# Optimization experiments

Measured on AMD Instinct MI355X. Metric: run time of the kernel, lower is better.

The kernel has to match this reference:

```python
import jax, jax.numpy as jnp
import numpy as np

SR = 48000
MIN_MIDI, MAX_MIDI = 30.0, 60.0
MIN_ALPHA, MAX_ALPHA = 0.2, 3.0
MIN_W, MAX_W = 100.0, 8000.0
MIN_Q, MAX_Q = 0.7071, 8.0
NOTE_ON_DUR = 0.125
OSC_SHAPE = 1.0
OSC_GAIN = 0.5
DIST_GAIN = 1.0
N = 524288


def setup_inputs() -> dict:
    key = jax.random.key(0)
    ks = jax.random.split(key, 5)
    return {
        "x": jax.random.normal(ks[0], (1, N), dtype=jnp.float32),
        "midi_f0_0to1": jax.random.uniform(ks[1], (1,), dtype=jnp.float32),
        "alpha_0to1": jax.random.uniform(ks[2], (1,), dtype=jnp.float32),
        "w_mod_sig": jax.random.uniform(ks[3], (1, N), dtype=jnp.float32),
        "q_mod_sig": jax.random.uniform(ks[4], (1, N), dtype=jnp.float32),
        "phase": jnp.zeros((1, 1), dtype=jnp.float32),
        "zi": jnp.zeros((1, 2), dtype=jnp.float32),
    }


def _tv_biquad(x, b, a, zi):
    # Time-varying biquad, direct-form II transposed.
    # x: [n], b: [n,3] (b0,b1,b2 normalized), a: [n,2] (a1,a2 normalized), zi: [2]
    def step(carry, inp):
        s1, s2 = carry
        xt, bt, at = inp
        y = bt[0] * xt + s1
        s1 = bt[1] * xt - at[0] * y + s2
        s2 = bt[2] * xt - at[1] * y
        return (s1, s2), y

    _, y = jax.lax.scan(step, (zi[0], zi[1]), (x, b, a))
    return y


def reference(x, midi_f0_0to1, alpha_0to1, w_mod_sig, q_mod_sig, phase, zi):
    n = x.shape[-1]
    # --- control mapping ---
    alpha = alpha_0to1 * (MAX_ALPHA - MIN_ALPHA) + MIN_ALPHA          # [1]
    midi_f0 = jnp.round(midi_f0_0to1 * (MAX_MIDI - MIN_MIDI) + MIN_MIDI)
    f0_hz = 440.0 * 2.0 ** ((midi_f0 - 69.0) / 12.0)                  # [1]
    t = jnp.arange(n, dtype=jnp.float32)
    # --- decaying note-on envelope raised to learned alpha ---
    env = jnp.clip(1.0 - t / (NOTE_ON_DUR * SR), 0.0, 1.0) ** alpha   # [n]
    # --- phase-accumulating saw/square morph oscillator ---
    arg = phase[0, 0] + 2.0 * jnp.pi * f0_hz * t / SR                 # [n]
    ph = jnp.mod(arg / (2.0 * jnp.pi), 1.0)
    saw = 2.0 * ph - 1.0
    sq = jnp.where(ph < 0.5, 1.0, -1.0)
    dry = OSC_GAIN * (OSC_SHAPE * sq + (1.0 - OSC_SHAPE) * saw) * env  # [n]
    # --- per-sample RBJ lowpass biquad coefficients ---
    w_hz = w_mod_sig[0] * (MAX_W - MIN_W) + MIN_W                     # [n]
    q = q_mod_sig[0] * (MAX_Q - MIN_Q) + MIN_Q                        # [n]
    w0 = 2.0 * jnp.pi * w_hz / SR
    cw, sw = jnp.cos(w0), jnp.sin(w0)
    af = sw / (2.0 * q)
    a0 = 1.0 + af
    b = jnp.stack([(1.0 - cw) / 2.0, 1.0 - cw, (1.0 - cw) / 2.0], axis=-1) / a0[:, None]
    a = jnp.stack([-2.0 * cw, 1.0 - af], axis=-1) / a0[:, None]
    # --- sequential time-varying filter + distortion ---
    y_a = _tv_biquad(dry, b, a, zi[0])                                # [n]
    wet = jnp.tanh(DIST_GAIN * y_a)[None, :]                          # [1, n]
    return wet
```

## Files before the change

### kernel.cpp

```cpp
#include <hip/hip_runtime.h>
#include <math.h>


#define LCHUNK 16

struct Aff { float m00,m01,m10,m11,c0,c1; };

__device__ __forceinline__ Aff aff_identity(){ return Aff{1.f,0.f,0.f,1.f,0.f,0.f}; }

__device__ __forceinline__ Aff aff_compose(const Aff& B, const Aff& A){
  Aff r;
  r.m00 = fmaf(B.m00, A.m00, B.m01*A.m10);
  r.m01 = fmaf(B.m00, A.m01, B.m01*A.m11);
  r.m10 = fmaf(B.m10, A.m00, B.m11*A.m10);
  r.m11 = fmaf(B.m10, A.m01, B.m11*A.m11);
  r.c0  = fmaf(B.m00, A.c0, fmaf(B.m01, A.c1, B.c0));
  r.c1  = fmaf(B.m10, A.c0, fmaf(B.m11, A.c1, B.c1));
  return r;
}

__device__ __forceinline__ Aff aff_shfl_up(const Aff& a, int delta){
  Aff r;
  r.m00 = __shfl_up(a.m00, delta, 64);
  r.m01 = __shfl_up(a.m01, delta, 64);
  r.m10 = __shfl_up(a.m10, delta, 64);
  r.m11 = __shfl_up(a.m11, delta, 64);
  r.c0  = __shfl_up(a.c0 , delta, 64);
  r.c1  = __shfl_up(a.c1 , delta, 64);
  return r;
}

__device__ __forceinline__ void coefs(float wv, float qv,
                                      float& na1, float& na2, float& b0, float& b1){
  float rev = fmaf(wv, 7900.0f/48000.0f, 100.0f/48000.0f);
  float cw = __builtin_amdgcn_cosf(rev);
  float sw = __builtin_amdgcn_sinf(rev);
  float qq = fmaf(qv, 8.0f - 0.7071f, 0.7071f);
  float af = sw * (0.5f * __builtin_amdgcn_rcpf(qq));
  float ia = __builtin_amdgcn_rcpf(1.0f + af);
  float t1 = 1.0f - cw;
  b1 = t1 * ia;
  b0 = 0.5f * b1;
  na1 = (cw + cw) * ia;
  na2 = (af - 1.0f) * ia;
}

__device__ __forceinline__ void get_controls(const float* midi01, const float* alpha01,
                                             const float* phasep,
                                             float& alpha, float& f0c, float& phase0){
  #pragma clang fp contract(off)
  alpha = alpha01[0]*2.8f + 0.2f;
  float md = rintf(midi01[0]*30.0f + 30.0f);
  float f0 = 440.0f * exp2f((md - 69.0f)/12.0f);
  f0c = 6.2831855f * f0;
  phase0 = phasep[0];
}

__device__ __forceinline__ float osc_dry(int i, float alpha, float f0c, float phase0){
  #pragma clang fp contract(off)
  float tf = (float)i;
  float u = 1.0f - tf/6000.0f;
  u = fminf(fmaxf(u, 0.0f), 1.0f);
  float env = powf(u, alpha);
  float arg = phase0 + (f0c*tf)/48000.0f;
  float d = arg/6.2831855f;
  float m = d - floorf(d);
  float sq = (m < 0.5f) ? 1.0f : -1.0f;
  return (0.5f*sq)*env;
}

__global__ __launch_bounds__(256) void k_pass1(const float* __restrict__ w,
    const float* __restrict__ qm, const float* __restrict__ midi01,
    const float* __restrict__ alpha01, const float* __restrict__ phasep,
    float4* __restrict__ Pf4, float2* __restrict__ Pf2, float4* __restrict__ Bt){
  const int tid = threadIdx.x;
  const int g = blockIdx.x*256 + tid;
  const int base = g * LCHUNK;
  float m00=1.f, m01=0.f, m10=0.f, m11=1.f, c0=0.f, c1=0.f;
  const bool has_dry = (base < 6000);
  float alpha=0.f, f0c=0.f, phase0=0.f;
  if (has_dry) get_controls(midi01, alpha01, phasep, alpha, f0c, phase0);
  const float4* w4p = reinterpret_cast<const float4*>(w + base);
  const float4* q4p = reinterpret_cast<const float4*>(qm + base);
  #pragma unroll
  for (int j=0;j<LCHUNK/4;j++){
    float4 w4 = w4p[j];
    float4 q4 = q4p[j];
    #pragma unroll
    for (int e=0;e<4;e++){
      float na1,na2,b0,b1;
      coefs((&w4.x)[e], (&q4.x)[e], na1,na2,b0,b1);
      float nm00 = fmaf(na1, m00, m10);
      float nm01 = fmaf(na1, m01, m11);
      m10 = na2*m00; m11 = na2*m01;
      m00 = nm00;   m01 = nm01;
      float nc0 = fmaf(na1, c0, c1);
      float nc1 = na2*c0;
      if (has_dry){
        float x = osc_dry(base + j*4 + e, alpha, f0c, phase0);
        nc0 = fmaf(fmaf(na1,b0,b1), x, nc0);
        nc1 = fmaf(fmaf(na2,b0,b0), x, nc1);
      }
      c0 = nc0; c1 = nc1;
    }
  }
  const int lane = tid & 63, wv = tid >> 6;
  Aff Tin{m00,m01,m10,m11,c0,c1};
  #pragma unroll
  for (int off=1; off<64; off<<=1){
    Aff P = aff_shfl_up(Tin, off);
    if (lane >= off) Tin = aff_compose(Tin, P);
  }
  __shared__ float wt[4][6];
  if (lane == 63){
    wt[wv][0]=Tin.m00; wt[wv][1]=Tin.m01; wt[wv][2]=Tin.m10;
    wt[wv][3]=Tin.m11; wt[wv][4]=Tin.c0;  wt[wv][5]=Tin.c1;
  }
  __syncthreads();
  Aff Wp = aff_identity();
  for (int j=0;j<wv;j++){
    Aff Wj{wt[j][0],wt[j][1],wt[j][2],wt[j][3],wt[j][4],wt[j][5]};
    Wp = aff_compose(Wj, Wp);
  }
  Aff Ex = aff_shfl_up(Tin, 1);
  if (lane == 0) Ex = aff_identity();
  Aff Epre = aff_compose(Ex, Wp);
  Pf4[g] = make_float4(Epre.m00, Epre.m01, Epre.m10, Epre.m11);
  Pf2[g] = make_float2(Epre.c0, Epre.c1);
  if (tid == 255){
    Aff Full = aff_compose(Tin, Wp);
    Bt[blockIdx.x*2+0] = make_float4(Full.m00, Full.m01, Full.m10, Full.m11);
    Bt[blockIdx.x*2+1] = make_float4(Full.c0, Full.c1, 0.f, 0.f);
  }
}

__global__ __launch_bounds__(256) void k_pass2(const float* __restrict__ w,
    const float* __restrict__ qm, const float* __restrict__ midi01,
    const float* __restrict__ alpha01, const float* __restrict__ phasep,
    const float* __restrict__ zi,
    const float4* __restrict__ Pf4, const float2* __restrict__ Pf2,
    const float4* __restrict__ Bt, float* __restrict__ out, int B){
  const int tid = threadIdx.x;
  const int blk = blockIdx.x;
  const int lane = tid & 63;
  __shared__ float2 stsh[128];
  __shared__ float wtot[6];
  const float z0 = zi[0], z1 = zi[1];
  if (tid < 128){
    Aff T = aff_identity();
    if (tid < B){
      float4 A4 = Bt[tid*2+0];
      float4 C4 = Bt[tid*2+1];
      T = Aff{A4.x,A4.y,A4.z,A4.w,C4.x,C4.y};
    }
    #pragma unroll
    for (int off=1; off<64; off<<=1){
      Aff P = aff_shfl_up(T, off);
      if (lane >= off) T = aff_compose(T, P);
    }
    if (tid == 63){
      wtot[0]=T.m00; wtot[1]=T.m01; wtot[2]=T.m10;
      wtot[3]=T.m11; wtot[4]=T.c0;  wtot[5]=T.c1;
    }
    __syncthreads();
    if (tid >= 64){
      Aff W0{wtot[0],wtot[1],wtot[2],wtot[3],wtot[4],wtot[5]};
      T = aff_compose(T, W0);
    }
    float s0 = fmaf(T.m00, z0, fmaf(T.m01, z1, T.c0));
    float s1 = fmaf(T.m10, z0, fmaf(T.m11, z1, T.c1));
    stsh[tid] = make_float2(s0, s1);
  } else {
    __syncthreads();
  }
  __syncthreads();
  const float2 e = (blk == 0) ? make_float2(z0, z1) : stsh[blk-1];
  const int g = blk*256 + tid;
  const int base = g * LCHUNK;
  float4 P4 = Pf4[g];
  float2 P2 = Pf2[g];
  float u1 = fmaf(P4.x, e.x, fmaf(P4.y, e.y, P2.x));
  float u2 = fmaf(P4.z, e.x, fmaf(P4.w, e.y, P2.y));
  const bool has_dry = (base < 6000);
  float alpha=0.f, f0c=0.f, phase0=0.f;
  if (has_dry) get_controls(midi01, alpha01, phasep, alpha, f0c, phase0);
  const float4* w4p = reinterpret_cast<const float4*>(w + base);
  const float4* q4p = reinterpret_cast<const float4*>(qm + base);
  float4* o4p = reinterpret_cast<float4*>(out + base);
  #pragma unroll
  for (int j=0;j<LCHUNK/4;j++){
    float4 w4 = w4p[j];
    float4 q4 = q4p[j];
    float4 ov;
    #pragma unroll
    for (int ecnt=0;ecnt<4;ecnt++){
      float na1,na2,b0,b1;
      coefs((&w4.x)[ecnt], (&q4.x)[ecnt], na1,na2,b0,b1);
      float x = 0.0f;
      if (has_dry) x = osc_dry(base + j*4 + ecnt, alpha, f0c, phase0);
      float y = fmaf(b0, x, u1);
      float nu1 = fmaf(b1, x, fmaf(na1, y, u2));
      float nu2 = fmaf(b0, x, na2*y);
      u1 = nu1; u2 = nu2;
      float ey = __expf(y + y);
      float r = __builtin_amdgcn_rcpf(ey + 1.0f);
      (&ov.x)[ecnt] = fmaf(-2.0f, r, 1.0f);
    }
    o4p[j] = ov;
  }
}

__global__ void k_naive(const float* __restrict__ w, const float* __restrict__ qm,
    const float* __restrict__ midi01, const float* __restrict__ alpha01,
    const float* __restrict__ phasep, const float* __restrict__ zi,
    float* __restrict__ out, int n){
  if (blockIdx.x != 0 || threadIdx.x != 0) return;
  float alpha,f0c,phase0; get_controls(midi01, alpha01, phasep, alpha, f0c, phase0);
  float u1 = zi[0], u2 = zi[1];
  for (int i=0;i<n;i++){
    float na1,na2,b0,b1;
    coefs(w[i], qm[i], na1,na2,b0,b1);
    float x = (i < 6000) ? osc_dry(i, alpha, f0c, phase0) : 0.0f;
    float y = fmaf(b0, x, u1);
    float nu1 = fmaf(b1, x, fmaf(na1, y, u2));
    float nu2 = fmaf(b0, x, na2*y);
    u1 = nu1; u2 = nu2;
    float ey = __expf(y + y);
    float r = __builtin_amdgcn_rcpf(ey + 1.0f);
    out[i] = fmaf(-2.0f, r, 1.0f);
  }
}

extern "C" void kernel_launch(void* const* d_in, const int* in_sizes, int n_in,
                              void* d_out, int out_size, void* d_ws, size_t ws_size,
                              hipStream_t stream) {
  const float* midi01  = (const float*)d_in[1];
  const float* alpha01 = (const float*)d_in[2];
  const float* w       = (const float*)d_in[3];
  const float* qm      = (const float*)d_in[4];
  const float* ph      = (const float*)d_in[5];
  const float* zi      = (const float*)d_in[6];
  float* out = (float*)d_out;
  const int n = in_sizes[0];
  const int G = n / LCHUNK;
  const int B = G / 256;
  const size_t pf4_bytes = (size_t)G * sizeof(float4);
  const size_t pf2_bytes = (size_t)G * sizeof(float2);
  const size_t bt_bytes  = (size_t)B * 2 * sizeof(float4);
  const size_t need = pf4_bytes + pf2_bytes + bt_bytes;

  if ((n % LCHUNK) != 0 || (G % 256) != 0 || B > 128 || ws_size < need) {
    k_naive<<<1, 64, 0, stream>>>(w, qm, midi01, alpha01, ph, zi, out, n);
    return;
  }
  float4* Pf4 = (float4*)d_ws;
  float2* Pf2 = (float2*)((char*)d_ws + pf4_bytes);
  float4* Bt  = (float4*)((char*)d_ws + pf4_bytes + pf2_bytes);

  k_pass1<<<dim3(B), dim3(256), 0, stream>>>(w, qm, midi01, alpha01, ph, Pf4, Pf2, Bt);
  k_pass2<<<dim3(B), dim3(256), 0, stream>>>(w, qm, midi01, alpha01, ph, zi,
                                             Pf4, Pf2, Bt, out, B);
}
```

Baseline: 87.75 us.

## Fuse two-pass biquad scan into one cooperative kernel with grid sync

Merges the two scan passes into one cooperative kernel. Per-sample coefficients and oscillator samples stay in registers across a grid.sync, so the second pass no longer reloads w/q, recomputes coefs and osc_dry, or round-trips per-thread prefix transforms through global memory. The cost is a cooperative launch with a grid-wide barrier and higher register pressure from 64 cached floats per thread. If the cooperative launch fails, it falls back to the serial naive kernel.

```diff
diff --git a/kernel.cpp b/kernel.cpp
--- a/kernel.cpp
+++ b/kernel.cpp
@@ -1,8 +1,12 @@
 #include <hip/hip_runtime.h>
+#include <hip/hip_cooperative_groups.h>
 #include <math.h>
 
 
+namespace cg = cooperative_groups;
+
 #define LCHUNK 16
+#define NBLK 128
 
 struct Aff { float m00,m01,m10,m11,c0,c1; };
 
@@ -31,7 +35,7 @@
 }
 
 __device__ __forceinline__ void coefs(float wv, float qv,
-                                      float& na1, float& na2, float& b0, float& b1){
+                                      float& na1, float& na2, float& b0){
   float rev = fmaf(wv, 7900.0f/48000.0f, 100.0f/48000.0f);
   float cw = __builtin_amdgcn_cosf(rev);
   float sw = __builtin_amdgcn_sinf(rev);
@@ -39,8 +43,7 @@
   float af = sw * (0.5f * __builtin_amdgcn_rcpf(qq));
   float ia = __builtin_amdgcn_rcpf(1.0f + af);
   float t1 = 1.0f - cw;
-  b1 = t1 * ia;
-  b0 = 0.5f * b1;
+  b0 = 0.5f * (t1 * ia);
   na1 = (cw + cw) * ia;
   na2 = (af - 1.0f) * ia;
 }
@@ -69,42 +72,56 @@
   return (0.5f*sq)*env;
 }
 
-__global__ __launch_bounds__(256) void k_pass1(const float* __restrict__ w,
+__global__ __launch_bounds__(256) void k_fused(const float* __restrict__ w,
     const float* __restrict__ qm, const float* __restrict__ midi01,
     const float* __restrict__ alpha01, const float* __restrict__ phasep,
-    float4* __restrict__ Pf4, float2* __restrict__ Pf2, float4* __restrict__ Bt){
+    const float* __restrict__ zi, float4* __restrict__ Bt,
+    float* __restrict__ out){
+  cg::grid_group grid = cg::this_grid();
   const int tid = threadIdx.x;
-  const int g = blockIdx.x*256 + tid;
+  const int blk = blockIdx.x;
+  const int lane = tid & 63, wv = tid >> 6;
+  const int g = blk*256 + tid;
   const int base = g * LCHUNK;
-  float m00=1.f, m01=0.f, m10=0.f, m11=1.f, c0=0.f, c1=0.f;
+
+  float na1s[LCHUNK], na2s[LCHUNK], b0s[LCHUNK], xs[LCHUNK];
   const bool has_dry = (base < 6000);
   float alpha=0.f, f0c=0.f, phase0=0.f;
   if (has_dry) get_controls(midi01, alpha01, phasep, alpha, f0c, phase0);
-  const float4* w4p = reinterpret_cast<const float4*>(w + base);
-  const float4* q4p = reinterpret_cast<const float4*>(qm + base);
+  {
+    const float4* w4p = reinterpret_cast<const float4*>(w + base);
+    const float4* q4p = reinterpret_cast<const float4*>(qm + base);
+    #pragma unroll
+    for (int j=0;j<LCHUNK/4;j++){
+      float4 w4 = w4p[j];
+      float4 q4 = q4p[j];
+      #pragma unroll
+      for (int e=0;e<4;e++){
+        int i = j*4 + e;
+        coefs((&w4.x)[e], (&q4.x)[e], na1s[i], na2s[i], b0s[i]);
+        xs[i] = has_dry ? osc_dry(base + i, alpha, f0c, phase0) : 0.0f;
+      }
+    }
+  }
+  float m00=1.f, m01=0.f, m10=0.f, m11=1.f, c0=0.f, c1=0.f;
   #pragma unroll
-  for (int j=0;j<LCHUNK/4;j++){
-    float4 w4 = w4p[j];
-    float4 q4 = q4p[j];
-    #pragma unroll
-    for (int e=0;e<4;e++){
-      float na1,na2,b0,b1;
-      coefs((&w4.x)[e], (&q4.x)[e], na1,na2,b0,b1);
-      float nm00 = fmaf(na1, m00, m10);
-      float nm01 = fmaf(na1, m01, m11);
-      m10 = na2*m00; m11 = na2*m01;
-      m00 = nm00;   m01 = nm01;
-      float nc0 = fmaf(na1, c0, c1);
-      float nc1 = na2*c0;
-      if (has_dry){
-        float x = osc_dry(base + j*4 + e, alpha, f0c, phase0);
-        nc0 = fmaf(fmaf(na1,b0,b1), x, nc0);
-        nc1 = fmaf(fmaf(na2,b0,b0), x, nc1);
-      }
-      c0 = nc0; c1 = nc1;
-    }
-  }
-  const int lane = tid & 63, wv = tid >> 6;
+  for (int i=0;i<LCHUNK;i++){
+    float na1 = na1s[i], na2 = na2s[i], b0 = b0s[i];
+    float nm00 = fmaf(na1, m00, m10);
+    float nm01 = fmaf(na1, m01, m11);
+    m10 = na2*m00; m11 = na2*m01;
+    m00 = nm00;   m01 = nm01;
+    float nc0 = fmaf(na1, c0, c1);
+    float nc1 = na2*c0;
+    if (has_dry){
+      float b1 = b0 + b0;
+      float x = xs[i];
+      nc0 = fmaf(fmaf(na1,b0,b1), x, nc0);
+      nc1 = fmaf(fmaf(na2,b0,b0), x, nc1);
+    }
+    c0 = nc0; c1 = nc1;
+  }
+
   Aff Tin{m00,m01,m10,m11,c0,c1};
   #pragma unroll
   for (int off=1; off<64; off<<=1){
@@ -125,34 +142,21 @@
   Aff Ex = aff_shfl_up(Tin, 1);
   if (lane == 0) Ex = aff_identity();
   Aff Epre = aff_compose(Ex, Wp);
-  Pf4[g] = make_float4(Epre.m00, Epre.m01, Epre.m10, Epre.m11);
-  Pf2[g] = make_float2(Epre.c0, Epre.c1);
   if (tid == 255){
     Aff Full = aff_compose(Tin, Wp);
-    Bt[blockIdx.x*2+0] = make_float4(Full.m00, Full.m01, Full.m10, Full.m11);
-    Bt[blockIdx.x*2+1] = make_float4(Full.c0, Full.c1, 0.f, 0.f);
-  }
-}
-
-__global__ __launch_bounds__(256) void k_pass2(const float* __restrict__ w,
-    const float* __restrict__ qm, const float* __restrict__ midi01,
-    const float* __restrict__ alpha01, const float* __restrict__ phasep,
-    const float* __restrict__ zi,
-    const float4* __restrict__ Pf4, const float2* __restrict__ Pf2,
-    const float4* __restrict__ Bt, float* __restrict__ out, int B){
-  const int tid = threadIdx.x;
-  const int blk = blockIdx.x;
-  const int lane = tid & 63;
-  __shared__ float2 stsh[128];
+    Bt[blk*2+0] = make_float4(Full.m00, Full.m01, Full.m10, Full.m11);
+    Bt[blk*2+1] = make_float4(Full.c0, Full.c1, 0.f, 0.f);
+  }
+
+  grid.sync();
+
+  __shared__ float2 stsh[NBLK];
   __shared__ float wtot[6];
   const float z0 = zi[0], z1 = zi[1];
-  if (tid < 128){
-    Aff T = aff_identity();
-    if (tid < B){
-      float4 A4 = Bt[tid*2+0];
-      float4 C4 = Bt[tid*2+1];
-      T = Aff{A4.x,A4.y,A4.z,A4.w,C4.x,C4.y};
-    }
+  if (tid < NBLK){
+    float4 A4 = Bt[tid*2+0];
+    float4 C4 = Bt[tid*2+1];
+    Aff T{A4.x,A4.y,A4.z,A4.w,C4.x,C4.y};
     #pragma unroll
     for (int off=1; off<64; off<<=1){
       Aff P = aff_shfl_up(T, off);
@@ -175,29 +179,19 @@
   }
   __syncthreads();
   const float2 e = (blk == 0) ? make_float2(z0, z1) : stsh[blk-1];
-  const int g = blk*256 + tid;
-  const int base = g * LCHUNK;
-  float4 P4 = Pf4[g];
-  float2 P2 = Pf2[g];
-  float u1 = fmaf(P4.x, e.x, fmaf(P4.y, e.y, P2.x));
-  float u2 = fmaf(P4.z, e.x, fmaf(P4.w, e.y, P2.y));
-  const bool has_dry = (base < 6000);
-  float alpha=0.f, f0c=0.f, phase0=0.f;
-  if (has_dry) get_controls(midi01, alpha01, phasep, alpha, f0c, phase0);
-  const float4* w4p = reinterpret_cast<const float4*>(w + base);
-  const float4* q4p = reinterpret_cast<const float4*>(qm + base);
+
+  float u1 = fmaf(Epre.m00, e.x, fmaf(Epre.m01, e.y, Epre.c0));
+  float u2 = fmaf(Epre.m10, e.x, fmaf(Epre.m11, e.y, Epre.c1));
   float4* o4p = reinterpret_cast<float4*>(out + base);
   #pragma unroll
   for (int j=0;j<LCHUNK/4;j++){
-    float4 w4 = w4p[j];
-    float4 q4 = q4p[j];
     float4 ov;
     #pragma unroll
     for (int ecnt=0;ecnt<4;ecnt++){
-      float na1,na2,b0,b1;
-      coefs((&w4.x)[ecnt], (&q4.x)[ecnt], na1,na2,b0,b1);
-      float x = 0.0f;
-      if (has_dry) x = osc_dry(base + j*4 + ecnt, alpha, f0c, phase0);
+      int i = j*4 + ecnt;
+      float na1 = na1s[i], na2 = na2s[i], b0 = b0s[i];
+      float b1 = b0 + b0;
+      float x = xs[i];
       float y = fmaf(b0, x, u1);
       float nu1 = fmaf(b1, x, fmaf(na1, y, u2));
       float nu2 = fmaf(b0, x, na2*y);
@@ -218,8 +212,9 @@
   float alpha,f0c,phase0; get_controls(midi01, alpha01, phasep, alpha, f0c, phase0);
   float u1 = zi[0], u2 = zi[1];
   for (int i=0;i<n;i++){
-    float na1,na2,b0,b1;
-    coefs(w[i], qm[i], na1,na2,b0,b1);
+    float na1,na2,b0;
+    coefs(w[i], qm[i], na1,na2,b0);
+    float b1 = b0 + b0;
     float x = (i < 6000) ? osc_dry(i, alpha, f0c, phase0) : 0.0f;
     float y = fmaf(b0, x, u1);
     float nu1 = fmaf(b1, x, fmaf(na1, y, u2));
@@ -244,20 +239,18 @@
   const int n = in_sizes[0];
   const int G = n / LCHUNK;
   const int B = G / 256;
-  const size_t pf4_bytes = (size_t)G * sizeof(float4);
-  const size_t pf2_bytes = (size_t)G * sizeof(float2);
-  const size_t bt_bytes  = (size_t)B * 2 * sizeof(float4);
-  const size_t need = pf4_bytes + pf2_bytes + bt_bytes;
-
-  if ((n % LCHUNK) != 0 || (G % 256) != 0 || B > 128 || ws_size < need) {
+  const size_t bt_bytes = (size_t)NBLK * 2 * sizeof(float4);
+
+  if ((n % (LCHUNK*256)) != 0 || B != NBLK || ws_size < bt_bytes) {
     k_naive<<<1, 64, 0, stream>>>(w, qm, midi01, alpha01, ph, zi, out, n);
     return;
   }
-  float4* Pf4 = (float4*)d_ws;
-  float2* Pf2 = (float2*)((char*)d_ws + pf4_bytes);
-  float4* Bt  = (float4*)((char*)d_ws + pf4_bytes + pf2_bytes);
-
-  k_pass1<<<dim3(B), dim3(256), 0, stream>>>(w, qm, midi01, alpha01, ph, Pf4, Pf2, Bt);
-  k_pass2<<<dim3(B), dim3(256), 0, stream>>>(w, qm, midi01, alpha01, ph, zi,
-                                             Pf4, Pf2, Bt, out, B);
-}
+  float4* Bt = (float4*)d_ws;
+  void* args[] = { (void*)&w, (void*)&qm, (void*)&midi01, (void*)&alpha01,
+                   (void*)&ph, (void*)&zi, (void*)&Bt, (void*)&out };
+  hipError_t err = hipLaunchCooperativeKernel((const void*)k_fused,
+                       dim3(NBLK), dim3(256), args, 0, stream);
+  if (err != hipSuccess) {
+    k_naive<<<1, 64, 0, stream>>>(w, qm, midi01, alpha01, ph, zi, out, n);
+  }
+}
```

Result: slower. 105.7 us (+20.4%).
